# Kernel optimization log

Measured on AMD Instinct MI355X. Metric: run time of the kernel, lower is better.

## Reference

```python
import jax, jax.numpy as jnp
import numpy as np

B, N, DIN, DOUT = 32, 1024, 256, 256


def setup_inputs() -> dict:
    key = jax.random.key(0)
    ks = jax.random.split(key, 7)
    s = 1.0 / np.sqrt(DIN)
    return {
        "x": jax.random.normal(ks[0], (B, N, DIN), dtype=jnp.float32),
        "Wq": jax.random.uniform(ks[1], (DOUT, DIN), minval=-s, maxval=s, dtype=jnp.float32),
        "bq": jax.random.uniform(ks[2], (DOUT,), minval=-s, maxval=s, dtype=jnp.float32),
        "Wk": jax.random.uniform(ks[3], (DOUT, DIN), minval=-s, maxval=s, dtype=jnp.float32),
        "bk": jax.random.uniform(ks[4], (DOUT,), minval=-s, maxval=s, dtype=jnp.float32),
        "Wv": jax.random.uniform(ks[5], (DOUT, DIN), minval=-s, maxval=s, dtype=jnp.float32),
        "bv": jax.random.uniform(ks[6], (DOUT,), minval=-s, maxval=s, dtype=jnp.float32),
    }


def reference(x, Wq, bq, Wk, bk, Wv, bv):
    # q, k, v: (B, N, Dout)
    q = jnp.einsum("bnd,od->bno", x, Wq) + bq
    k = jnp.einsum("bnd,od->bno", x, Wk) + bk
    v = jnp.einsum("bnd,od->bno", x, Wv) + bv
    # logits: (B, N, N) = q @ k^T per batch
    logits = jnp.einsum("bnd,bmd->bnm", q, k)
    # NOTE: softmax over the BATCH dim (axis=0), as in the original module
    attn = jax.nn.softmax(logits, axis=0)
    out = jnp.einsum("bnm,bmd->bnd", attn, v)  # (B, N, Dout)
    return out
```

## Files before the change

kernel.cpp:

```cpp
#include <hip/hip_runtime.h>

typedef __bf16 bf16x8 __attribute__((ext_vector_type(8)));
typedef __bf16 bf16x4 __attribute__((ext_vector_type(4)));
typedef float  f32x4  __attribute__((ext_vector_type(4)));

#define BK 64

__device__ __forceinline__ void g2l16(const void* g, void* l) {
    __builtin_amdgcn_global_load_lds((const __attribute__((address_space(1))) void*)g,
                                     (__attribute__((address_space(3))) void*)l, 16, 0, 0);
}


__global__ __launch_bounds__(256)
void gemm_proj(const __bf16* __restrict__ A, const __bf16* __restrict__ Wb,
               __bf16* __restrict__ qkv, const float* __restrict__ bpack)
{
    __shared__ __align__(16) __bf16 smem[128 * 128];
    __bf16* As = smem;
    __bf16* Bs = smem + 128 * BK;

    const int tid  = threadIdx.x;
    const int w    = tid >> 6;
    const int lane = tid & 63;
    const int quad = lane >> 4;
    const int l16  = lane & 15;
    const int wm   = w & 1;
    const int wn   = w >> 1;

    const int m0 = blockIdx.x * 128;
    const int n0 = blockIdx.y * 128;
    const int z  = blockIdx.z;

    const __bf16* Bb   = Wb + (size_t)z * 131072;
    const float*  bias = bpack + z * 256;

    const int srow = (w << 3) + (lane >> 3);
    const int scol = ((lane & 7) ^ (lane >> 3)) << 3;
    char* ldsA = (char*)As + (size_t)w * 1024;
    char* ldsB = (char*)Bs + (size_t)w * 1024;

    const __bf16* Ag = A  + (size_t)(m0 + srow) * 256 + scol;
    const __bf16* Bg = Bb + (size_t)(n0 + srow) * 256 + scol;

    f32x4 acc[4][4] = {};

    for (int k0 = 0; k0 < 256; k0 += BK) {
        __syncthreads();
        #pragma unroll
        for (int c = 0; c < 4; c++)
            g2l16(Ag + (size_t)(c * 32) * 256 + k0, ldsA + c * 4096);
        #pragma unroll
        for (int c = 0; c < 4; c++)
            g2l16(Bg + (size_t)(c * 32) * 256 + k0, ldsB + c * 4096);
        __syncthreads();

        #pragma unroll
        for (int kk = 0; kk < BK; kk += 32) {
            const int ub = kk >> 3;
            bf16x8 a[4], b[4];
            #pragma unroll
            for (int mt = 0; mt < 4; mt++) {
                const int row = wm * 64 + mt * 16 + l16;
                const int cp  = ((quad + ub) ^ (row & 7)) << 3;
                a[mt] = *(const bf16x8*)&As[row * BK + cp];
            }
            #pragma unroll
            for (int nt = 0; nt < 4; nt++) {
                const int row = wn * 64 + nt * 16 + l16;
                const int cp  = ((quad + ub) ^ (row & 7)) << 3;
                b[nt] = *(const bf16x8*)&Bs[row * BK + cp];
            }
            #pragma unroll
            for (int mt = 0; mt < 4; mt++)
                #pragma unroll
                for (int nt = 0; nt < 4; nt++)
                    acc[mt][nt] = __builtin_amdgcn_mfma_f32_16x16x32_bf16(
                        a[mt], b[nt], acc[mt][nt], 0, 0, 0);
        }
    }

    __syncthreads();
    if (z < 2) {
        #pragma unroll
        for (int mt = 0; mt < 4; mt++) {
            const int rl = wm * 64 + mt * 16 + quad * 4;
            #pragma unroll
            for (int nt = 0; nt < 4; nt++) {
                const int cl = wn * 64 + nt * 16 + l16;
                const float bn = bias[n0 + cl];
                #pragma unroll
                for (int r = 0; r < 4; r++) {
                    const int row = rl + r;
                    smem[row * 128 + ((((cl >> 3) ^ (row & 7)) << 3) | (cl & 7))] =
                        (__bf16)(acc[mt][nt][r] + bn);
                }
            }
        }
        __syncthreads();
        __bf16* C = qkv + (size_t)z * 8388608;
        #pragma unroll
        for (int i = 0; i < 8; i++) {
            const int c   = tid + i * 256;
            const int row = c >> 4, u = c & 15;
            *(bf16x8*)&C[(size_t)(m0 + row) * 256 + n0 + u * 8] =
                *(const bf16x8*)&smem[row * 128 + ((u ^ (row & 7)) << 3)];
        }
    } else {
        #pragma unroll
        for (int mt = 0; mt < 4; mt++) {
            const int ml = wm * 64 + mt * 16 + quad * 4;
            #pragma unroll
            for (int nt = 0; nt < 4; nt++) {
                const int dl = wn * 64 + nt * 16 + l16;
                const float bn = bias[n0 + dl];
                bf16x4 pk;
                #pragma unroll
                for (int r = 0; r < 4; r++) pk[r] = (__bf16)(acc[mt][nt][r] + bn);
                *(bf16x4*)&smem[dl * 128 + ((((ml >> 3) ^ (dl & 7)) << 3) | (ml & 7))] = pk;
            }
        }
        __syncthreads();
        __bf16* C = qkv + 2 * 8388608;
        const int bidx = m0 >> 10, mbase = m0 & 1023;
        #pragma unroll
        for (int i = 0; i < 8; i++) {
            const int c  = tid + i * 256;
            const int dl = c >> 4, u = c & 15;
            *(bf16x8*)&C[(size_t)bidx * 262144 + (size_t)(n0 + dl) * 1024 + mbase + u * 8] =
                *(const bf16x8*)&smem[dl * 128 + ((u ^ (dl & 7)) << 3)];
        }
    }
}

__global__ __launch_bounds__(256)
void gemm_logits(const __bf16* __restrict__ Q, const __bf16* __restrict__ Km,
                 __bf16* __restrict__ E)
{
    __shared__ __align__(16) __bf16 smem[128 * 128];
    __bf16* As = smem;
    __bf16* Bs = smem + 128 * BK;

    const int tid  = threadIdx.x;
    const int w    = tid >> 6;
    const int lane = tid & 63;
    const int quad = lane >> 4;
    const int l16  = lane & 15;
    const int wm   = w & 1;
    const int wn   = w >> 1;

    const int id = blockIdx.x;
    const int x  = id & 7, s = id >> 3;
    const int z  = x + ((s >> 6) << 3);
    const int t  = s & 63;
    const int m0 = (t & 7) * 128;
    const int n0 = (t >> 3) * 128;

    const __bf16* Ab = Q  + (size_t)z * 262144;
    const __bf16* Bb = Km + (size_t)z * 262144;

    const int srow = (w << 3) + (lane >> 3);
    const int scol = ((lane & 7) ^ (lane >> 3)) << 3;
    char* ldsA = (char*)As + (size_t)w * 1024;
    char* ldsB = (char*)Bs + (size_t)w * 1024;

    const __bf16* Ag = Ab + (size_t)(m0 + srow) * 256 + scol;
    const __bf16* Bg = Bb + (size_t)(n0 + srow) * 256 + scol;

    f32x4 acc[4][4] = {};

    for (int k0 = 0; k0 < 256; k0 += BK) {
        __syncthreads();
        #pragma unroll
        for (int c = 0; c < 4; c++)
            g2l16(Ag + (size_t)(c * 32) * 256 + k0, ldsA + c * 4096);
        #pragma unroll
        for (int c = 0; c < 4; c++)
            g2l16(Bg + (size_t)(c * 32) * 256 + k0, ldsB + c * 4096);
        __syncthreads();

        #pragma unroll
        for (int kk = 0; kk < BK; kk += 32) {
            const int ub = kk >> 3;
            bf16x8 a[4], b[4];
            #pragma unroll
            for (int mt = 0; mt < 4; mt++) {
                const int row = wm * 64 + mt * 16 + l16;
                const int cp  = ((quad + ub) ^ (row & 7)) << 3;
                a[mt] = *(const bf16x8*)&As[row * BK + cp];
            }
            #pragma unroll
            for (int nt = 0; nt < 4; nt++) {
                const int row = wn * 64 + nt * 16 + l16;
                const int cp  = ((quad + ub) ^ (row & 7)) << 3;
                b[nt] = *(const bf16x8*)&Bs[row * BK + cp];
            }
            #pragma unroll
            for (int mt = 0; mt < 4; mt++)
                #pragma unroll
                for (int nt = 0; nt < 4; nt++)
                    acc[mt][nt] = __builtin_amdgcn_mfma_f32_16x16x32_bf16(
                        a[mt], b[nt], acc[mt][nt], 0, 0, 0);
        }
    }

    __syncthreads();
    #pragma unroll
    for (int mt = 0; mt < 4; mt++) {
        const int rl = wm * 64 + mt * 16 + quad * 4;
        #pragma unroll
        for (int nt = 0; nt < 4; nt++) {
            const int cl = wn * 64 + nt * 16 + l16;
            #pragma unroll
            for (int r = 0; r < 4; r++) {
                const int row = rl + r;
                smem[row * 128 + ((((cl >> 3) ^ (row & 7)) << 3) | (cl & 7))] =
                    (__bf16)__expf(acc[mt][nt][r]);
            }
        }
    }
    __syncthreads();
    __bf16* C = E + (size_t)z * 1048576;
    #pragma unroll
    for (int i = 0; i < 8; i++) {
        const int c   = tid + i * 256;
        const int row = c >> 4, u = c & 15;
        *(bf16x8*)&C[(size_t)(m0 + row) * 1024 + n0 + u * 8] =
            *(const bf16x8*)&smem[row * 128 + ((u ^ (row & 7)) << 3)];
    }
}

__global__ __launch_bounds__(256)
void sum_rcp(const __bf16* __restrict__ E, __bf16* __restrict__ rcpS)
{
    const size_t p = (size_t)blockIdx.x * 256 + threadIdx.x;
    const bf16x8* E8 = (const bf16x8*)E;
    float s[8] = {0.f, 0.f, 0.f, 0.f, 0.f, 0.f, 0.f, 0.f};
    #pragma unroll
    for (int b = 0; b < 32; b++) {
        const bf16x8 e = E8[(size_t)b * 131072 + p];
        #pragma unroll
        for (int j = 0; j < 8; j++) s[j] += (float)e[j];
    }
    bf16x8 o;
    #pragma unroll
    for (int j = 0; j < 8; j++) o[j] = (__bf16)__builtin_amdgcn_rcpf(s[j]);
    ((bf16x8*)rcpS)[p] = o;
}

__global__ __launch_bounds__(256)
void gemm_pv(const __bf16* __restrict__ E, const __bf16* __restrict__ rcpS,
             const __bf16* __restrict__ vT, float* __restrict__ out)
{
    __shared__ __align__(16) __bf16 As[128 * BK];
    __shared__ __align__(16) __bf16 Bs[64 * BK];

    const int tid  = threadIdx.x;
    const int w    = tid >> 6;
    const int lane = tid & 63;
    const int quad = lane >> 4;
    const int l16  = lane & 15;
    const int wm   = w & 1;
    const int wn   = w >> 1;

    const int id = blockIdx.x;
    const int x  = id & 7, s = id >> 3;
    const int z  = x + ((s >> 5) << 3);
    const int t  = s & 31;
    const int m0 = (t & 7) * 128;
    const int n0 = (t >> 3) * 64;

    const __bf16* Eb = E  + (size_t)z * 1048576;
    const __bf16* Vb = vT + (size_t)z * 262144;
    float*        Ob = out + (size_t)z * 262144;

    const int srow = (w << 3) + (lane >> 3);
    const int scol = ((lane & 7) ^ (lane >> 3)) << 3;
    char* ldsAw = (char*)As + w * 1024 + lane * 16;
    char* ldsB  = (char*)Bs + (size_t)w * 1024;

    const __bf16* Ag = Eb   + (size_t)(m0 + srow) * 1024 + scol;
    const __bf16* Rg = rcpS + (size_t)(m0 + srow) * 1024 + scol;
    const __bf16* Bg = Vb   + (size_t)(n0 + srow) * 1024 + scol;

    f32x4 acc[4][2] = {};

    for (int k0 = 0; k0 < 1024; k0 += BK) {
        __syncthreads();
        #pragma unroll
        for (int c = 0; c < 4; c++) {
            const bf16x8 e  = *(const bf16x8*)(Ag + (size_t)(c * 32) * 1024 + k0);
            const bf16x8 rs = *(const bf16x8*)(Rg + (size_t)(c * 32) * 1024 + k0);
            bf16x8 o;
            #pragma unroll
            for (int j = 0; j < 8; j++) o[j] = (__bf16)((float)e[j] * (float)rs[j]);
            *(bf16x8*)(ldsAw + c * 4096) = o;
        }
        #pragma unroll
        for (int c = 0; c < 2; c++)
            g2l16(Bg + (size_t)(c * 32) * 1024 + k0, ldsB + c * 4096);
        __syncthreads();

        #pragma unroll
        for (int kk = 0; kk < BK; kk += 32) {
            const int ub = kk >> 3;
            bf16x8 a[4], b[2];
            #pragma unroll
            for (int mt = 0; mt < 4; mt++) {
                const int row = wm * 64 + mt * 16 + l16;
                const int cp  = ((quad + ub) ^ (row & 7)) << 3;
                a[mt] = *(const bf16x8*)&As[row * BK + cp];
            }
            #pragma unroll
            for (int nt = 0; nt < 2; nt++) {
                const int row = wn * 32 + nt * 16 + l16;
                const int cp  = ((quad + ub) ^ (row & 7)) << 3;
                b[nt] = *(const bf16x8*)&Bs[row * BK + cp];
            }
            #pragma unroll
            for (int mt = 0; mt < 4; mt++)
                #pragma unroll
                for (int nt = 0; nt < 2; nt++)
                    acc[mt][nt] = __builtin_amdgcn_mfma_f32_16x16x32_bf16(
                        a[mt], b[nt], acc[mt][nt], 0, 0, 0);
        }
    }

    #pragma unroll
    for (int mt = 0; mt < 4; mt++) {
        const int mb = m0 + wm * 64 + mt * 16 + quad * 4;
        #pragma unroll
        for (int nt = 0; nt < 2; nt++) {
            const int n = n0 + wn * 32 + nt * 16 + l16;
            #pragma unroll
            for (int r = 0; r < 4; r++)
                Ob[(size_t)(mb + r) * 256 + n] = acc[mt][nt][r];
        }
    }
}

__global__ __launch_bounds__(256)
void cvt_all(const float* __restrict__ x,
             const float* __restrict__ Wq, const float* __restrict__ Wk,
             const float* __restrict__ Wv,
             const float* __restrict__ bq, const float* __restrict__ bk,
             const float* __restrict__ bv,
             __bf16* __restrict__ xb, __bf16* __restrict__ Wqb,
             float* __restrict__ bpack)
{
    const int i = blockIdx.x * 256 + threadIdx.x;
    if (i < 1073152) {
        const float* s; __bf16* d; int off;
        if (i < 1048576)      { s = x;  d = xb;            off = i; }
        else if (i < 1056768) { s = Wq; d = Wqb;           off = i - 1048576; }
        else if (i < 1064960) { s = Wk; d = Wqb + 131072;  off = i - 1056768; }
        else                  { s = Wv; d = Wqb + 262144;  off = i - 1064960; }
        const float4* s4 = (const float4*)s;
        const float4 f0 = s4[off * 2], f1 = s4[off * 2 + 1];
        bf16x8 o;
        o[0] = (__bf16)f0.x; o[1] = (__bf16)f0.y; o[2] = (__bf16)f0.z; o[3] = (__bf16)f0.w;
        o[4] = (__bf16)f1.x; o[5] = (__bf16)f1.y; o[6] = (__bf16)f1.z; o[7] = (__bf16)f1.w;
        ((bf16x8*)d)[off] = o;
    } else if (i < 1073344) {
        const int j = i - 1073152;
        const int sel = j >> 6, jj = j & 63;
        const float* s = sel == 0 ? bq : (sel == 1 ? bk : bv);
        ((float4*)bpack)[j] = ((const float4*)s)[jj];
    }
}

extern "C" void kernel_launch(void* const* d_in, const int* in_sizes, int n_in,
                              void* d_out, int out_size, void* d_ws, size_t ws_size,
                              hipStream_t stream)
{
    const float* x  = (const float*)d_in[0];
    const float* Wq = (const float*)d_in[1];
    const float* bq = (const float*)d_in[2];
    const float* Wk = (const float*)d_in[3];
    const float* bk = (const float*)d_in[4];
    const float* Wv = (const float*)d_in[5];
    const float* bv = (const float*)d_in[6];
    float* out = (float*)d_out;

    char* ws = (char*)d_ws;
    __bf16* rcpS = (__bf16*)ws;
    __bf16* xb   = (__bf16*)(ws + (2u  << 20));
    __bf16* qkv  = (__bf16*)(ws + (18u << 20));
    __bf16* E    = (__bf16*)(ws + (66u << 20));
    __bf16* Wqb  = (__bf16*)(ws + (130u << 20));
    float*  bpack = (float*)(ws + (130u << 20) + (1u << 20));

    cvt_all<<<4194, 256, 0, stream>>>(x, Wq, Wk, Wv, bq, bk, bv, xb, Wqb, bpack);

    gemm_proj<<<dim3(256, 2, 3), 256, 0, stream>>>(xb, Wqb, qkv, bpack);

    gemm_logits<<<2048, 256, 0, stream>>>(qkv, qkv + 8388608, E);

    sum_rcp<<<512, 256, 0, stream>>>(E, rcpS);

    gemm_pv<<<1024, 256, 0, stream>>>(E, rcpS, qkv + 2 * 8388608, out);
}
```

Measured before the change: 197.4 us.

## Double-buffer LDS tiles in logits and PV GEMMs to overlap loads with MFMA

Both the logits GEMM and the PV GEMM now use two LDS buffers per operand. The next K-tile is prefetched (async global-to-LDS for B and Q/K, register staging for the normalized E tile) while MFMAs run on the current tile, and one of the two barriers per iteration is removed. The intent is to hide global memory latency behind compute. In exchange, LDS use grows (64KB for logits, 48KB for PV) and register pressure rises from the staged e/rs vectors, which may reduce occupancy.

```diff
diff --git a/kernel.cpp b/kernel.cpp
--- a/kernel.cpp
+++ b/kernel.cpp
@@ -137,9 +137,7 @@
 void gemm_logits(const __bf16* __restrict__ Q, const __bf16* __restrict__ Km,
                  __bf16* __restrict__ E)
 {
-    __shared__ __align__(16) __bf16 smem[128 * 128];
-    __bf16* As = smem;
-    __bf16* Bs = smem + 128 * BK;
+    __shared__ __align__(16) __bf16 smem[32768];
 
     const int tid  = threadIdx.x;
     const int w    = tid >> 6;
@@ -152,33 +150,45 @@
     const int id = blockIdx.x;
     const int x  = id & 7, s = id >> 3;
     const int z  = x + ((s >> 6) << 3);
-    const int t  = s & 63;
-    const int m0 = (t & 7) * 128;
-    const int n0 = (t >> 3) * 128;
+    const int t_ = s & 63;
+    const int m0 = (t_ & 7) * 128;
+    const int n0 = (t_ >> 3) * 128;
 
     const __bf16* Ab = Q  + (size_t)z * 262144;
     const __bf16* Bb = Km + (size_t)z * 262144;
 
     const int srow = (w << 3) + (lane >> 3);
     const int scol = ((lane & 7) ^ (lane >> 3)) << 3;
-    char* ldsA = (char*)As + (size_t)w * 1024;
-    char* ldsB = (char*)Bs + (size_t)w * 1024;
 
     const __bf16* Ag = Ab + (size_t)(m0 + srow) * 256 + scol;
     const __bf16* Bg = Bb + (size_t)(n0 + srow) * 256 + scol;
 
     f32x4 acc[4][4] = {};
 
-    for (int k0 = 0; k0 < 256; k0 += BK) {
-        __syncthreads();
-        #pragma unroll
-        for (int c = 0; c < 4; c++)
-            g2l16(Ag + (size_t)(c * 32) * 256 + k0, ldsA + c * 4096);
-        #pragma unroll
-        for (int c = 0; c < 4; c++)
-            g2l16(Bg + (size_t)(c * 32) * 256 + k0, ldsB + c * 4096);
-        __syncthreads();
-
+    #pragma unroll
+    for (int c = 0; c < 4; c++)
+        g2l16(Ag + (size_t)(c * 32) * 256, (char*)smem + w * 1024 + c * 4096);
+    #pragma unroll
+    for (int c = 0; c < 4; c++)
+        g2l16(Bg + (size_t)(c * 32) * 256, (char*)smem + 32768 + w * 1024 + c * 4096);
+    __syncthreads();
+
+    for (int t = 0; t < 4; t++) {
+        const int cur = t & 1;
+        if (t < 3) {
+            const int k1 = (t + 1) * BK;
+            const int nb = cur ^ 1;
+            #pragma unroll
+            for (int c = 0; c < 4; c++)
+                g2l16(Ag + (size_t)(c * 32) * 256 + k1,
+                      (char*)smem + nb * 16384 + w * 1024 + c * 4096);
+            #pragma unroll
+            for (int c = 0; c < 4; c++)
+                g2l16(Bg + (size_t)(c * 32) * 256 + k1,
+                      (char*)smem + 32768 + nb * 16384 + w * 1024 + c * 4096);
+        }
+        const __bf16* As = smem + cur * 8192;
+        const __bf16* Bs = smem + 16384 + cur * 8192;
         #pragma unroll
         for (int kk = 0; kk < BK; kk += 32) {
             const int ub = kk >> 3;
@@ -202,9 +212,9 @@
                     acc[mt][nt] = __builtin_amdgcn_mfma_f32_16x16x32_bf16(
                         a[mt], b[nt], acc[mt][nt], 0, 0, 0);
         }
-    }
-
-    __syncthreads();
+        __syncthreads();
+    }
+
     #pragma unroll
     for (int mt = 0; mt < 4; mt++) {
         const int rl = wm * 64 + mt * 16 + quad * 4;
@@ -252,8 +262,7 @@
 void gemm_pv(const __bf16* __restrict__ E, const __bf16* __restrict__ rcpS,
              const __bf16* __restrict__ vT, float* __restrict__ out)
 {
-    __shared__ __align__(16) __bf16 As[128 * BK];
-    __shared__ __align__(16) __bf16 Bs[64 * BK];
+    __shared__ __align__(16) __bf16 smem[24576];
 
     const int tid  = threadIdx.x;
     const int w    = tid >> 6;
@@ -266,9 +275,9 @@
     const int id = blockIdx.x;
     const int x  = id & 7, s = id >> 3;
     const int z  = x + ((s >> 5) << 3);
-    const int t  = s & 31;
-    const int m0 = (t & 7) * 128;
-    const int n0 = (t >> 3) * 64;
+    const int t_ = s & 31;
+    const int m0 = (t_ & 7) * 128;
+    const int n0 = (t_ >> 3) * 64;
 
     const __bf16* Eb = E  + (size_t)z * 1048576;
     const __bf16* Vb = vT + (size_t)z * 262144;
@@ -276,31 +285,49 @@
 
     const int srow = (w << 3) + (lane >> 3);
     const int scol = ((lane & 7) ^ (lane >> 3)) << 3;
-    char* ldsAw = (char*)As + w * 1024 + lane * 16;
-    char* ldsB  = (char*)Bs + (size_t)w * 1024;
 
     const __bf16* Ag = Eb   + (size_t)(m0 + srow) * 1024 + scol;
     const __bf16* Rg = rcpS + (size_t)(m0 + srow) * 1024 + scol;
     const __bf16* Bg = Vb   + (size_t)(n0 + srow) * 1024 + scol;
 
     f32x4 acc[4][2] = {};
-
-    for (int k0 = 0; k0 < 1024; k0 += BK) {
-        __syncthreads();
-        #pragma unroll
-        for (int c = 0; c < 4; c++) {
-            const bf16x8 e  = *(const bf16x8*)(Ag + (size_t)(c * 32) * 1024 + k0);
-            const bf16x8 rs = *(const bf16x8*)(Rg + (size_t)(c * 32) * 1024 + k0);
-            bf16x8 o;
-            #pragma unroll
-            for (int j = 0; j < 8; j++) o[j] = (__bf16)((float)e[j] * (float)rs[j]);
-            *(bf16x8*)(ldsAw + c * 4096) = o;
-        }
-        #pragma unroll
-        for (int c = 0; c < 2; c++)
-            g2l16(Bg + (size_t)(c * 32) * 1024 + k0, ldsB + c * 4096);
-        __syncthreads();
-
+    bf16x8 e[4], rs[4];
+
+    #pragma unroll
+    for (int c = 0; c < 4; c++) {
+        e[c]  = *(const bf16x8*)(Ag + (size_t)(c * 32) * 1024);
+        rs[c] = *(const bf16x8*)(Rg + (size_t)(c * 32) * 1024);
+    }
+    #pragma unroll
+    for (int c = 0; c < 2; c++)
+        g2l16(Bg + (size_t)(c * 32) * 1024, (char*)smem + 32768 + w * 1024 + c * 4096);
+    #pragma unroll
+    for (int c = 0; c < 4; c++) {
+        bf16x8 o;
+        #pragma unroll
+        for (int j = 0; j < 8; j++) o[j] = (__bf16)((float)e[c][j] * (float)rs[c][j]);
+        *(bf16x8*)((char*)smem + w * 1024 + lane * 16 + c * 4096) = o;
+    }
+    __syncthreads();
+
+    for (int t = 0; t < 16; t++) {
+        const int cur = t & 1;
+        const int nb  = cur ^ 1;
+        if (t < 15) {
+            const int k1 = (t + 1) * BK;
+            #pragma unroll
+            for (int c = 0; c < 4; c++) {
+                e[c]  = *(const bf16x8*)(Ag + (size_t)(c * 32) * 1024 + k1);
+                rs[c] = *(const bf16x8*)(Rg + (size_t)(c * 32) * 1024 + k1);
+            }
+            #pragma unroll
+            for (int c = 0; c < 2; c++)
+                g2l16(Bg + (size_t)(c * 32) * 1024 + k1,
+                      (char*)smem + 32768 + nb * 8192 + w * 1024 + c * 4096);
+        }
+
+        const __bf16* As = smem + cur * 8192;
+        const __bf16* Bs = smem + 16384 + cur * 4096;
         #pragma unroll
         for (int kk = 0; kk < BK; kk += 32) {
             const int ub = kk >> 3;
@@ -324,6 +351,17 @@
                     acc[mt][nt] = __builtin_amdgcn_mfma_f32_16x16x32_bf16(
                         a[mt], b[nt], acc[mt][nt], 0, 0, 0);
         }
+
+        if (t < 15) {
+            #pragma unroll
+            for (int c = 0; c < 4; c++) {
+                bf16x8 o;
+                #pragma unroll
+                for (int j = 0; j < 8; j++) o[j] = (__bf16)((float)e[c][j] * (float)rs[c][j]);
+                *(bf16x8*)((char*)smem + nb * 16384 + w * 1024 + lane * 16 + c * 4096) = o;
+            }
+        }
+        __syncthreads();
     }
 
     #pragma unroll
```

Measured after the change: 196.5 us. Within noise of the previous version (-0.4%).

## Load MFMA operands directly from global memory in logits and PV GEMMs

Applied to the files above, without the earlier changes.

Removes LDS staging and the block-level barriers from the logits GEMM and the PV GEMM. Each wave now reads its MFMA A/B fragments straight from global memory into registers, with a partial unroll of the K loop. This drops shared-memory round trips and syncs, but operands are no longer shared across waves within a block. Each wave re-fetches data that was previously loaded once per block, so it relies on L1/L2 caching to absorb the extra, less coalesced global traffic.

```diff
diff --git a/kernel.cpp b/kernel.cpp
--- a/kernel.cpp
+++ b/kernel.cpp
@@ -10,7 +10,6 @@
     __builtin_amdgcn_global_load_lds((const __attribute__((address_space(1))) void*)g,
                                      (__attribute__((address_space(3))) void*)l, 16, 0, 0);
 }
-
 
 __global__ __launch_bounds__(256)
 void gemm_proj(const __bf16* __restrict__ A, const __bf16* __restrict__ Wb,
@@ -138,8 +137,6 @@
                  __bf16* __restrict__ E)
 {
     __shared__ __align__(16) __bf16 smem[128 * 128];
-    __bf16* As = smem;
-    __bf16* Bs = smem + 128 * BK;
 
     const int tid  = threadIdx.x;
     const int w    = tid >> 6;
@@ -152,59 +149,34 @@
     const int id = blockIdx.x;
     const int x  = id & 7, s = id >> 3;
     const int z  = x + ((s >> 6) << 3);
-    const int t  = s & 63;
-    const int m0 = (t & 7) * 128;
-    const int n0 = (t >> 3) * 128;
-
-    const __bf16* Ab = Q  + (size_t)z * 262144;
-    const __bf16* Bb = Km + (size_t)z * 262144;
-
-    const int srow = (w << 3) + (lane >> 3);
-    const int scol = ((lane & 7) ^ (lane >> 3)) << 3;
-    char* ldsA = (char*)As + (size_t)w * 1024;
-    char* ldsB = (char*)Bs + (size_t)w * 1024;
-
-    const __bf16* Ag = Ab + (size_t)(m0 + srow) * 256 + scol;
-    const __bf16* Bg = Bb + (size_t)(n0 + srow) * 256 + scol;
+    const int t_ = s & 63;
+    const int m0 = (t_ & 7) * 128;
+    const int n0 = (t_ >> 3) * 128;
+
+    const __bf16* Qa = Q  + (size_t)z * 262144
+                     + (size_t)(m0 + wm * 64 + l16) * 256 + quad * 8;
+    const __bf16* Ka = Km + (size_t)z * 262144
+                     + (size_t)(n0 + wn * 64 + l16) * 256 + quad * 8;
 
     f32x4 acc[4][4] = {};
 
-    for (int k0 = 0; k0 < 256; k0 += BK) {
-        __syncthreads();
-        #pragma unroll
-        for (int c = 0; c < 4; c++)
-            g2l16(Ag + (size_t)(c * 32) * 256 + k0, ldsA + c * 4096);
-        #pragma unroll
-        for (int c = 0; c < 4; c++)
-            g2l16(Bg + (size_t)(c * 32) * 256 + k0, ldsB + c * 4096);
-        __syncthreads();
-
-        #pragma unroll
-        for (int kk = 0; kk < BK; kk += 32) {
-            const int ub = kk >> 3;
-            bf16x8 a[4], b[4];
-            #pragma unroll
-            for (int mt = 0; mt < 4; mt++) {
-                const int row = wm * 64 + mt * 16 + l16;
-                const int cp  = ((quad + ub) ^ (row & 7)) << 3;
-                a[mt] = *(const bf16x8*)&As[row * BK + cp];
-            }
-            #pragma unroll
-            for (int nt = 0; nt < 4; nt++) {
-                const int row = wn * 64 + nt * 16 + l16;
-                const int cp  = ((quad + ub) ^ (row & 7)) << 3;
-                b[nt] = *(const bf16x8*)&Bs[row * BK + cp];
-            }
-            #pragma unroll
-            for (int mt = 0; mt < 4; mt++)
-                #pragma unroll
-                for (int nt = 0; nt < 4; nt++)
-                    acc[mt][nt] = __builtin_amdgcn_mfma_f32_16x16x32_bf16(
-                        a[mt], b[nt], acc[mt][nt], 0, 0, 0);
-        }
-    }
-
-    __syncthreads();
+    #pragma unroll 2
+    for (int k = 0; k < 256; k += 32) {
+        bf16x8 a[4], b[4];
+        #pragma unroll
+        for (int mt = 0; mt < 4; mt++)
+            a[mt] = *(const bf16x8*)(Qa + mt * (16 * 256) + k);
+        #pragma unroll
+        for (int nt = 0; nt < 4; nt++)
+            b[nt] = *(const bf16x8*)(Ka + nt * (16 * 256) + k);
+        #pragma unroll
+        for (int mt = 0; mt < 4; mt++)
+            #pragma unroll
+            for (int nt = 0; nt < 4; nt++)
+                acc[mt][nt] = __builtin_amdgcn_mfma_f32_16x16x32_bf16(
+                    a[mt], b[nt], acc[mt][nt], 0, 0, 0);
+    }
+
     #pragma unroll
     for (int mt = 0; mt < 4; mt++) {
         const int rl = wm * 64 + mt * 16 + quad * 4;
@@ -252,9 +224,6 @@
 void gemm_pv(const __bf16* __restrict__ E, const __bf16* __restrict__ rcpS,
              const __bf16* __restrict__ vT, float* __restrict__ out)
 {
-    __shared__ __align__(16) __bf16 As[128 * BK];
-    __shared__ __align__(16) __bf16 Bs[64 * BK];
-
     const int tid  = threadIdx.x;
     const int w    = tid >> 6;
     const int lane = tid & 63;
@@ -266,64 +235,39 @@
     const int id = blockIdx.x;
     const int x  = id & 7, s = id >> 3;
     const int z  = x + ((s >> 5) << 3);
-    const int t  = s & 31;
-    const int m0 = (t & 7) * 128;
-    const int n0 = (t >> 3) * 64;
-
-    const __bf16* Eb = E  + (size_t)z * 1048576;
-    const __bf16* Vb = vT + (size_t)z * 262144;
-    float*        Ob = out + (size_t)z * 262144;
-
-    const int srow = (w << 3) + (lane >> 3);
-    const int scol = ((lane & 7) ^ (lane >> 3)) << 3;
-    char* ldsAw = (char*)As + w * 1024 + lane * 16;
-    char* ldsB  = (char*)Bs + (size_t)w * 1024;
-
-    const __bf16* Ag = Eb   + (size_t)(m0 + srow) * 1024 + scol;
-    const __bf16* Rg = rcpS + (size_t)(m0 + srow) * 1024 + scol;
-    const __bf16* Bg = Vb   + (size_t)(n0 + srow) * 1024 + scol;
+    const int t_ = s & 31;
+    const int m0 = (t_ & 7) * 128;
+    const int n0 = (t_ >> 3) * 64;
+
+    const int arow = m0 + wm * 64 + l16;
+    const __bf16* Ea = E    + (size_t)z * 1048576 + (size_t)arow * 1024 + quad * 8;
+    const __bf16* Ra = rcpS +                       (size_t)arow * 1024 + quad * 8;
+    const __bf16* Va = vT   + (size_t)z * 262144
+                     + (size_t)(n0 + wn * 32 + l16) * 1024 + quad * 8;
+    float* Ob = out + (size_t)z * 262144;
 
     f32x4 acc[4][2] = {};
 
-    for (int k0 = 0; k0 < 1024; k0 += BK) {
-        __syncthreads();
-        #pragma unroll
-        for (int c = 0; c < 4; c++) {
-            const bf16x8 e  = *(const bf16x8*)(Ag + (size_t)(c * 32) * 1024 + k0);
-            const bf16x8 rs = *(const bf16x8*)(Rg + (size_t)(c * 32) * 1024 + k0);
-            bf16x8 o;
-            #pragma unroll
-            for (int j = 0; j < 8; j++) o[j] = (__bf16)((float)e[j] * (float)rs[j]);
-            *(bf16x8*)(ldsAw + c * 4096) = o;
-        }
-        #pragma unroll
-        for (int c = 0; c < 2; c++)
-            g2l16(Bg + (size_t)(c * 32) * 1024 + k0, ldsB + c * 4096);
-        __syncthreads();
-
-        #pragma unroll
-        for (int kk = 0; kk < BK; kk += 32) {
-            const int ub = kk >> 3;
-            bf16x8 a[4], b[2];
-            #pragma unroll
-            for (int mt = 0; mt < 4; mt++) {
-                const int row = wm * 64 + mt * 16 + l16;
-                const int cp  = ((quad + ub) ^ (row & 7)) << 3;
-                a[mt] = *(const bf16x8*)&As[row * BK + cp];
-            }
-            #pragma unroll
-            for (int nt = 0; nt < 2; nt++) {
-                const int row = wn * 32 + nt * 16 + l16;
-                const int cp  = ((quad + ub) ^ (row & 7)) << 3;
-                b[nt] = *(const bf16x8*)&Bs[row * BK + cp];
-            }
-            #pragma unroll
-            for (int mt = 0; mt < 4; mt++)
-                #pragma unroll
-                for (int nt = 0; nt < 2; nt++)
-                    acc[mt][nt] = __builtin_amdgcn_mfma_f32_16x16x32_bf16(
-                        a[mt], b[nt], acc[mt][nt], 0, 0, 0);
-        }
+    #pragma unroll 2
+    for (int k = 0; k < 1024; k += 32) {
+        bf16x8 a[4], b[2];
+        #pragma unroll
+        for (int mt = 0; mt < 4; mt++) {
+            const bf16x8 e  = *(const bf16x8*)(Ea + mt * (16 * 1024) + k);
+            const bf16x8 rs = *(const bf16x8*)(Ra + mt * (16 * 1024) + k);
+            #pragma unroll
+            for (int j = 0; j < 8; j++)
+                a[mt][j] = (__bf16)((float)e[j] * (float)rs[j]);
+        }
+        #pragma unroll
+        for (int nt = 0; nt < 2; nt++)
+            b[nt] = *(const bf16x8*)(Va + nt * (16 * 1024) + k);
+        #pragma unroll
+        for (int mt = 0; mt < 4; mt++)
+            #pragma unroll
+            for (int nt = 0; nt < 2; nt++)
+                acc[mt][nt] = __builtin_amdgcn_mfma_f32_16x16x32_bf16(
+                    a[mt], b[nt], acc[mt][nt], 0, 0, 0);
     }
 
     #pragma unroll
```

After: 362.7 us. +83.8%, slower.

## Normalize softmax in place and triple-buffer async loads in PV GEMM

Applied to the files above, without the earlier changes.

The batch-axis softmax reduction kernel now keeps all 32 batch values in registers, computes the reciprocal sum, and writes the normalized probabilities back into E in place, so the separate reciprocal buffer is gone. The PV GEMM then loads pre-normalized E directly with global-to-LDS async copies into a 3-stage ring buffer, using vmcnt waits and one barrier per iteration. This replaces the synchronous register loads with a per-element multiply on every tile. The cost is an extra full write of the 64MB E tensor in the reduction kernel, plus 32 vector registers per thread holding the batch values.

```diff
diff --git a/kernel.cpp b/kernel.cpp
--- a/kernel.cpp
+++ b/kernel.cpp
@@ -152,9 +152,9 @@
     const int id = blockIdx.x;
     const int x  = id & 7, s = id >> 3;
     const int z  = x + ((s >> 6) << 3);
-    const int t  = s & 63;
-    const int m0 = (t & 7) * 128;
-    const int n0 = (t >> 3) * 128;
+    const int t_ = s & 63;
+    const int m0 = (t_ & 7) * 128;
+    const int n0 = (t_ >> 3) * 128;
 
     const __bf16* Ab = Q  + (size_t)z * 262144;
     const __bf16* Bb = Km + (size_t)z * 262144;
@@ -231,29 +231,35 @@
 }
 
 __global__ __launch_bounds__(256)
-void sum_rcp(const __bf16* __restrict__ E, __bf16* __restrict__ rcpS)
+void softmax_norm(__bf16* __restrict__ E)
 {
     const size_t p = (size_t)blockIdx.x * 256 + threadIdx.x;
-    const bf16x8* E8 = (const bf16x8*)E;
+    bf16x8* E8 = (bf16x8*)E;
+    bf16x8 e[32];
+    #pragma unroll
+    for (int b = 0; b < 32; b++) e[b] = E8[(size_t)b * 131072 + p];
     float s[8] = {0.f, 0.f, 0.f, 0.f, 0.f, 0.f, 0.f, 0.f};
     #pragma unroll
+    for (int b = 0; b < 32; b++)
+        #pragma unroll
+        for (int j = 0; j < 8; j++) s[j] += (float)e[b][j];
+    float rs[8];
+    #pragma unroll
+    for (int j = 0; j < 8; j++) rs[j] = __builtin_amdgcn_rcpf(s[j]);
+    #pragma unroll
     for (int b = 0; b < 32; b++) {
-        const bf16x8 e = E8[(size_t)b * 131072 + p];
-        #pragma unroll
-        for (int j = 0; j < 8; j++) s[j] += (float)e[j];
-    }
-    bf16x8 o;
-    #pragma unroll
-    for (int j = 0; j < 8; j++) o[j] = (__bf16)__builtin_amdgcn_rcpf(s[j]);
-    ((bf16x8*)rcpS)[p] = o;
+        bf16x8 o = e[b];
+        #pragma unroll
+        for (int j = 0; j < 8; j++) o[j] = (__bf16)((float)o[j] * rs[j]);
+        E8[(size_t)b * 131072 + p] = o;
+    }
 }
 
 __global__ __launch_bounds__(256)
-void gemm_pv(const __bf16* __restrict__ E, const __bf16* __restrict__ rcpS,
-             const __bf16* __restrict__ vT, float* __restrict__ out)
-{
-    __shared__ __align__(16) __bf16 As[128 * BK];
-    __shared__ __align__(16) __bf16 Bs[64 * BK];
+void gemm_pv(const __bf16* __restrict__ En, const __bf16* __restrict__ vT,
+             float* __restrict__ out)
+{
+    __shared__ __align__(16) __bf16 smem[3 * 12288];
 
     const int tid  = threadIdx.x;
     const int w    = tid >> 6;
@@ -266,41 +272,48 @@
     const int id = blockIdx.x;
     const int x  = id & 7, s = id >> 3;
     const int z  = x + ((s >> 5) << 3);
-    const int t  = s & 31;
-    const int m0 = (t & 7) * 128;
-    const int n0 = (t >> 3) * 64;
-
-    const __bf16* Eb = E  + (size_t)z * 1048576;
+    const int t_ = s & 31;
+    const int m0 = (t_ & 7) * 128;
+    const int n0 = (t_ >> 3) * 64;
+
+    const __bf16* Eb = En + (size_t)z * 1048576;
     const __bf16* Vb = vT + (size_t)z * 262144;
     float*        Ob = out + (size_t)z * 262144;
 
     const int srow = (w << 3) + (lane >> 3);
     const int scol = ((lane & 7) ^ (lane >> 3)) << 3;
-    char* ldsAw = (char*)As + w * 1024 + lane * 16;
-    char* ldsB  = (char*)Bs + (size_t)w * 1024;
-
-    const __bf16* Ag = Eb   + (size_t)(m0 + srow) * 1024 + scol;
-    const __bf16* Rg = rcpS + (size_t)(m0 + srow) * 1024 + scol;
-    const __bf16* Bg = Vb   + (size_t)(n0 + srow) * 1024 + scol;
+
+    const __bf16* Ag = Eb + (size_t)(m0 + srow) * 1024 + scol;
+    const __bf16* Bg = Vb + (size_t)(n0 + srow) * 1024 + scol;
 
     f32x4 acc[4][2] = {};
 
-    for (int k0 = 0; k0 < 1024; k0 += BK) {
-        __syncthreads();
-        #pragma unroll
-        for (int c = 0; c < 4; c++) {
-            const bf16x8 e  = *(const bf16x8*)(Ag + (size_t)(c * 32) * 1024 + k0);
-            const bf16x8 rs = *(const bf16x8*)(Rg + (size_t)(c * 32) * 1024 + k0);
-            bf16x8 o;
-            #pragma unroll
-            for (int j = 0; j < 8; j++) o[j] = (__bf16)((float)e[j] * (float)rs[j]);
-            *(bf16x8*)(ldsAw + c * 4096) = o;
-        }
+    auto STAGE = [&](int buf, int k0) {
+        char* base = (char*)smem + buf * 24576;
+        #pragma unroll
+        for (int c = 0; c < 4; c++)
+            g2l16(Ag + (size_t)(c * 32) * 1024 + k0, base + w * 1024 + c * 4096);
         #pragma unroll
         for (int c = 0; c < 2; c++)
-            g2l16(Bg + (size_t)(c * 32) * 1024 + k0, ldsB + c * 4096);
-        __syncthreads();
-
+            g2l16(Bg + (size_t)(c * 32) * 1024 + k0, base + 16384 + w * 1024 + c * 4096);
+    };
+
+    STAGE(0, 0);
+    STAGE(1, 64);
+
+    for (int t = 0; t < 16; t++) {
+        if (t < 15) {
+            asm volatile("s_waitcnt vmcnt(6)" ::: "memory");
+        } else {
+            asm volatile("s_waitcnt vmcnt(0)" ::: "memory");
+        }
+        __builtin_amdgcn_sched_barrier(0);
+        __builtin_amdgcn_s_barrier();
+
+        if (t + 2 < 16) STAGE((t + 2) % 3, (t + 2) * BK);
+
+        const __bf16* As = smem + (t % 3) * 12288;
+        const __bf16* Bs = As + 8192;
         #pragma unroll
         for (int kk = 0; kk < BK; kk += 32) {
             const int ub = kk >> 3;
@@ -383,7 +396,6 @@
     float* out = (float*)d_out;
 
     char* ws = (char*)d_ws;
-    __bf16* rcpS = (__bf16*)ws;
     __bf16* xb   = (__bf16*)(ws + (2u  << 20));
     __bf16* qkv  = (__bf16*)(ws + (18u << 20));
     __bf16* E    = (__bf16*)(ws + (66u << 20));
@@ -396,7 +408,7 @@
 
     gemm_logits<<<2048, 256, 0, stream>>>(qkv, qkv + 8388608, E);
 
-    sum_rcp<<<512, 256, 0, stream>>>(E, rcpS);
-
-    gemm_pv<<<1024, 256, 0, stream>>>(E, rcpS, qkv + 2 * 8388608, out);
-}
+    softmax_norm<<<512, 256, 0, stream>>>(E);
+
+    gemm_pv<<<1024, 256, 0, stream>>>(E, qkv + 2 * 8388608, out);
+}
```

Result: faster. 191.8 us (-2.8%).
